# Optimization experiments

Hardware: AMD Instinct MI355X
Metric: run time of the kernel (lower is better)

## Reference

```python
import jax, jax.numpy as jnp
import numpy as np
import math

N_EMBD = 1024
N_HEAD = 16
HEAD_DIM = N_EMBD // N_HEAD


def setup_inputs() -> dict:
    key = jax.random.key(0)
    k_x, k_w1, k_b1, k_w2, k_b2 = jax.random.split(key, 5)
    B, T = 2, 2048
    x = jax.random.normal(k_x, (B, T, N_EMBD), dtype=jnp.float32)
    # ln1: Linear(n_embd, 3*n_embd); weights stored as [in, out] for x @ W
    W_qkv = jax.random.normal(k_w1, (N_EMBD, 3 * N_EMBD), dtype=jnp.float32) * 0.02
    b_qkv = jax.random.normal(k_b1, (3 * N_EMBD,), dtype=jnp.float32) * 0.02
    # ln2: Linear(n_embd, n_embd)
    W_out = jax.random.normal(k_w2, (N_EMBD, N_EMBD), dtype=jnp.float32) * 0.02
    b_out = jax.random.normal(k_b2, (N_EMBD,), dtype=jnp.float32) * 0.02
    return {"x": x, "W_qkv": W_qkv, "b_qkv": b_qkv, "W_out": W_out, "b_out": b_out}


def reference(x, W_qkv, b_qkv, W_out, b_out):
    B, T, C = x.shape
    qkv = x @ W_qkv + b_qkv                      # [B,T,3C]
    q, k, v = jnp.split(qkv, 3, axis=-1)
    # reshape to heads: [B, H, T, D]
    def to_heads(t):
        return t.reshape(B, T, N_HEAD, HEAD_DIM).transpose(0, 2, 1, 3)
    Q, K, V = to_heads(q), to_heads(k), to_heads(v)
    # NOTE: scale is 1/sqrt(n_head), as in the source (not sqrt(head_dim));
    # NOTE: no causal mask is applied, faithfully matching the source forward.
    scale = 1.0 / math.sqrt(N_HEAD)
    scores = jnp.einsum('bhqd,bhkd->bhqk', Q, K) * scale  # [B,H,T,T]
    attn = jax.nn.softmax(scores, axis=-1)
    out = jnp.einsum('bhqk,bhkd->bhqd', attn, V)          # [B,H,T,D]
    out = out.transpose(0, 2, 1, 3).reshape(B, T, C)
    # dropout = 0.0 -> identity (eval mode)
    return out @ W_out + b_out
```

## Files before the change

kernel.cpp:

```cpp
#include <hip/hip_runtime.h>
#include <hip/hip_bf16.h>
#include <stdint.h>

typedef __bf16 bf16_t;
typedef __bf16 bf16x8 __attribute__((ext_vector_type(8)));
typedef float  f32x4  __attribute__((ext_vector_type(4)));

#define AS1 __attribute__((address_space(1)))
#define AS3 __attribute__((address_space(3)))

__device__ __forceinline__ void gload16(const bf16_t* g, char* l) {
  __builtin_amdgcn_global_load_lds((AS1 const void*)(uintptr_t)g, (AS3 void*)l, 16, 0, 0);
}
__device__ __forceinline__ int swz8(int r) { return (r & 7) ^ ((r >> 2) & 6); }

#define C2S 0.36067376022224085f

__global__ void cvt_f32_bf16(const float* __restrict__ in, bf16_t* __restrict__ out, int n4) {
  int i = blockIdx.x * blockDim.x + threadIdx.x;
  if (i >= n4) return;
  float4 v = reinterpret_cast<const float4*>(in)[i];
  union { bf16_t h[4]; unsigned long long u; } r;
  r.h[0] = (bf16_t)v.x; r.h[1] = (bf16_t)v.y; r.h[2] = (bf16_t)v.z; r.h[3] = (bf16_t)v.w;
  reinterpret_cast<unsigned long long*>(out)[i] = r.u;
}

__global__ void trans_cvt(const float* __restrict__ W, bf16_t* __restrict__ Wt, int K, int N) {
  __shared__ float tile[32][33];
  const int kb = blockIdx.x * 32, nb = blockIdx.y * 32;
  const int tx = threadIdx.x, ty = threadIdx.y;
#pragma unroll
  for (int i = 0; i < 32; i += 8)
    tile[ty + i][tx] = W[(size_t)(kb + ty + i) * N + nb + tx];
  __syncthreads();
#pragma unroll
  for (int i = 0; i < 32; i += 8)
    Wt[(size_t)(nb + ty + i) * K + kb + tx] = (bf16_t)tile[tx][ty + i];
}

__global__ __launch_bounds__(256) void gemm_bt(
    const bf16_t* __restrict__ A, const bf16_t* __restrict__ Bt,
    const float* __restrict__ bias,
    bf16_t* __restrict__ outb, bf16_t* __restrict__ vtb, float* __restrict__ outf,
    int M, int N, int K, int ldo, int mode) {
  __shared__ bf16_t lA[128 * 32];
  __shared__ bf16_t lB[128 * 32];
  const int tid = threadIdx.x;
  const int wave = tid >> 6, lane = tid & 63;
  const int lr = lane & 15, lg = lane >> 4;
  const int ntiles = N >> 7;
  const int bid = (blockIdx.x & 7) * ((int)gridDim.x >> 3) + (blockIdx.x >> 3);
  const int bn = bid % ntiles, bm = bid / ntiles;
  const int m0 = bm * 128, n0 = bn * 128;
  const int wr = wave >> 1, wc = wave & 1;
  f32x4 acc[4][4] = {};

  for (int k0 = 0; k0 < K; k0 += 32) {
    __syncthreads();
#pragma unroll
    for (int it = 0; it < 2; ++it) {
      const int wbase = it * 256 + wave * 64;
      const int lam = wbase + lane;
      const int row = lam >> 2;
      const int colb = ((lam & 3) << 4) ^ (((row >> 1) & 3) << 4);
      gload16(A  + (size_t)(m0 + row) * K + k0 + (colb >> 1), (char*)lA + wbase * 16);
      gload16(Bt + (size_t)(n0 + row) * K + k0 + (colb >> 1), (char*)lB + wbase * 16);
    }
    __syncthreads();

    bf16x8 af[4], bfv[4];
#pragma unroll
    for (int mi = 0; mi < 4; ++mi) {
      const int row = wr * 64 + mi * 16 + lr;
      af[mi] = *reinterpret_cast<const bf16x8*>(
          (const char*)lA + row * 64 + ((lg * 16) ^ (((row >> 1) & 3) << 4)));
    }
#pragma unroll
    for (int ni = 0; ni < 4; ++ni) {
      const int row = wc * 64 + ni * 16 + lr;
      bfv[ni] = *reinterpret_cast<const bf16x8*>(
          (const char*)lB + row * 64 + ((lg * 16) ^ (((row >> 1) & 3) << 4)));
    }
    __builtin_amdgcn_s_setprio(1);
#pragma unroll
    for (int mi = 0; mi < 4; ++mi)
#pragma unroll
      for (int ni = 0; ni < 4; ++ni)
        acc[mi][ni] = __builtin_amdgcn_mfma_f32_16x16x32_bf16(af[mi], bfv[ni], acc[mi][ni], 0, 0, 0);
    __builtin_amdgcn_s_setprio(0);
  }

#pragma unroll
  for (int mi = 0; mi < 4; ++mi) {
#pragma unroll
    for (int ni = 0; ni < 4; ++ni) {
      const int col = n0 + wc * 64 + ni * 16 + lr;
      const float bv = bias[col];
      const int rg0 = m0 + wr * 64 + mi * 16 + lg * 4;
      if (mode == 1 && col >= 2048) {
        const int colv = col - 2048;
        const int dd = colv & 63, hh = colv >> 6;
        const int bb = rg0 >> 11, t = rg0 & 2047;
        union { bf16_t h4[4]; unsigned long long u; } pk;
#pragma unroll
        for (int r = 0; r < 4; ++r) pk.h4[r] = (bf16_t)(acc[mi][ni][r] + bv);
        *reinterpret_cast<unsigned long long*>(
            vtb + (size_t)(bb * 16 + hh) * 131072 + (size_t)dd * 2048 + t) = pk.u;
      } else {
        const float sc = (mode == 1 && col < 1024) ? C2S : 1.f;
#pragma unroll
        for (int r = 0; r < 4; ++r) {
          const float v = (acc[mi][ni][r] + bv) * sc;
          if (mode == 2) outf[(size_t)(rg0 + r) * ldo + col] = v;
          else           outb[(size_t)(rg0 + r) * ldo + col] = (bf16_t)v;
        }
      }
    }
  }
}

__global__ __launch_bounds__(512) void attn_fwd(
    const bf16_t* __restrict__ qkv2,
    const bf16_t* __restrict__ vT,
    bf16_t* __restrict__ a0, bf16_t* __restrict__ a1,
    float* __restrict__ lbuf) {
  __shared__ bf16_t lds[2][8192];
  const int tid = threadIdx.x;
  const int wave = tid >> 6, lane = tid & 63;
  const int lr = lane & 15, lg = lane >> 4;
  const int id = blockIdx.x;
  const int xcd = id & 7, slot = id >> 3;
  const int bh = xcd * 4 + (slot & 3);
  const int rest = slot >> 2;
  const int qb = rest & 7, kvh = rest >> 3;
  const int b = bh >> 4, h = bh & 15;

  const int q0 = qb * 256 + wave * 32;
  const bf16_t* Qp = qkv2 + (size_t)(b * 2048 + q0) * 2048 + h * 64;
  bf16x8 qf[2][2];
#pragma unroll
  for (int hx = 0; hx < 2; ++hx) {
    qf[hx][0] = *reinterpret_cast<const bf16x8*>(Qp + (size_t)(hx * 16 + lr) * 2048 + lg * 8);
    qf[hx][1] = *reinterpret_cast<const bf16x8*>(Qp + (size_t)(hx * 16 + lr) * 2048 + 32 + lg * 8);
  }

  const int kr = tid >> 3;
  const int ks = (tid & 7) ^ swz8(kr);
  const bf16_t* Ksrc = qkv2 + (size_t)(b * 2048 + kvh * 1024 + kr) * 2048 + 1024 + h * 64 + ks * 8;
  const bf16_t* Vsrc = vT + (size_t)bh * 131072 + (size_t)kr * 2048 + kvh * 1024 + ks * 8;

  auto stage = [&](int buf, int kb) {
    char* base = (char*)&lds[buf][0] + wave * 1024;
    gload16(Ksrc + (size_t)kb * 131072, base);
    gload16(Vsrc + (size_t)kb * 64, base + 8192);
  };

  int kofs[4][2], vofs[4][2];
#pragma unroll
  for (int t = 0; t < 4; ++t) {
    const int kk = 32 * (t >> 1) + 8 * (lr >> 2) + 4 * (t & 1) + (lr & 3);
    const int sw = swz8(kk) << 4;
    kofs[t][0] = (kk << 7) + ((lg * 16) ^ sw);
    kofs[t][1] = (kk << 7) + ((64 + lg * 16) ^ sw);
  }
#pragma unroll
  for (int nc = 0; nc < 4; ++nc) {
    const int vr = nc * 16 + lr;
    const int sw = swz8(vr) << 4;
    vofs[nc][0] = 8192 + (vr << 7) + ((lg * 16) ^ sw);
    vofs[nc][1] = 8192 + (vr << 7) + ((64 + lg * 16) ^ sw);
  }

  f32x4 acc[2][4] = {};
  f32x4 accl[2] = {};
  bf16x8 ones;
#pragma unroll
  for (int j = 0; j < 8; ++j) ones[j] = (bf16_t)1.0f;

  int cur = 0;
  stage(0, 0);
  __syncthreads();

  for (int kb = 0; kb < 16; ++kb) {
    if (kb < 15) stage(cur ^ 1, kb + 1);
    const char* bK = (const char*)&lds[cur][0];

    f32x4 s[2][4];
#pragma unroll
    for (int t = 0; t < 4; ++t) {
      const bf16x8 k0 = *reinterpret_cast<const bf16x8*>(bK + kofs[t][0]);
      const bf16x8 k1 = *reinterpret_cast<const bf16x8*>(bK + kofs[t][1]);
#pragma unroll
      for (int hx = 0; hx < 2; ++hx) {
        f32x4 z = {0.f, 0.f, 0.f, 0.f};
        z = __builtin_amdgcn_mfma_f32_16x16x32_bf16(k0, qf[hx][0], z, 0, 0, 0);
        s[hx][t] = __builtin_amdgcn_mfma_f32_16x16x32_bf16(k1, qf[hx][1], z, 0, 0, 0);
      }
    }

    bf16x8 pa[2][2];
#pragma unroll
    for (int hx = 0; hx < 2; ++hx) {
      float p[16];
#pragma unroll
      for (int t = 0; t < 4; ++t)
#pragma unroll
        for (int r = 0; r < 4; ++r)
          p[t * 4 + r] = __builtin_amdgcn_exp2f(s[hx][t][r]);
#pragma unroll
      for (int j = 0; j < 8; ++j) { pa[hx][0][j] = (bf16_t)p[j]; pa[hx][1][j] = (bf16_t)p[8 + j]; }
    }

    __builtin_amdgcn_s_setprio(1);
#pragma unroll
    for (int hx = 0; hx < 2; ++hx) {
      accl[hx] = __builtin_amdgcn_mfma_f32_16x16x32_bf16(pa[hx][0], ones, accl[hx], 0, 0, 0);
      accl[hx] = __builtin_amdgcn_mfma_f32_16x16x32_bf16(pa[hx][1], ones, accl[hx], 0, 0, 0);
    }

#pragma unroll
    for (int nc = 0; nc < 4; ++nc) {
      const bf16x8 v0 = *reinterpret_cast<const bf16x8*>(bK + vofs[nc][0]);
      const bf16x8 v1 = *reinterpret_cast<const bf16x8*>(bK + vofs[nc][1]);
#pragma unroll
      for (int hx = 0; hx < 2; ++hx) {
        acc[hx][nc] = __builtin_amdgcn_mfma_f32_16x16x32_bf16(pa[hx][0], v0, acc[hx][nc], 0, 0, 0);
        acc[hx][nc] = __builtin_amdgcn_mfma_f32_16x16x32_bf16(pa[hx][1], v1, acc[hx][nc], 0, 0, 0);
      }
    }
    __builtin_amdgcn_s_setprio(0);

    __syncthreads();
    cur ^= 1;
  }

  bf16_t* ap = kvh ? a1 : a0;
#pragma unroll
  for (int hx = 0; hx < 2; ++hx) {
#pragma unroll
    for (int r = 0; r < 4; ++r) {
      const float lf = 1.f / accl[hx][r];
      const int qg = q0 + hx * 16 + lg * 4 + r;
      bf16_t* op = ap + (size_t)(b * 2048 + qg) * 1024 + h * 64 + lr;
#pragma unroll
      for (int nc = 0; nc < 4; ++nc) op[nc * 16] = (bf16_t)(acc[hx][nc][r] * lf);
      if (lr == 0)
        lbuf[(size_t)(kvh * 4096 + b * 2048 + qg) * 16 + h] = accl[hx][r];
    }
  }
}

__global__ void attn_reduce(const bf16_t* __restrict__ a0, const bf16_t* __restrict__ a1,
                            const float* __restrict__ lbuf, bf16_t* __restrict__ aout) {
  const int i = blockIdx.x * 256 + threadIdx.x;
  const int r = i >> 7, h = (i & 127) >> 3;
  const float l0 = lbuf[(size_t)r * 16 + h];
  const float l1 = lbuf[(size_t)(4096 + r) * 16 + h];
  const float inv = 1.f / (l0 + l1);
  const float w0 = l0 * inv, w1 = l1 * inv;
  const bf16x8 v0 = reinterpret_cast<const bf16x8*>(a0)[i];
  const bf16x8 v1 = reinterpret_cast<const bf16x8*>(a1)[i];
  bf16x8 o;
#pragma unroll
  for (int j = 0; j < 8; ++j) o[j] = (bf16_t)(w0 * (float)v0[j] + w1 * (float)v1[j]);
  reinterpret_cast<bf16x8*>(aout)[i] = o;
}

extern "C" void kernel_launch(void* const* d_in, const int* in_sizes, int n_in,
                              void* d_out, int out_size, void* d_ws, size_t ws_size,
                              hipStream_t stream) {
  (void)in_sizes; (void)n_in; (void)out_size; (void)ws_size;
  const float* x    = (const float*)d_in[0];
  const float* Wqkv = (const float*)d_in[1];
  const float* bqkv = (const float*)d_in[2];
  const float* Wout = (const float*)d_in[3];
  const float* bout = (const float*)d_in[4];
  float* out = (float*)d_out;

  char* ws = (char*)d_ws;
  bf16_t* xb    = (bf16_t*)(ws);
  bf16_t* a0    = (bf16_t*)(ws);
  bf16_t* wqkvT = (bf16_t*)(ws + 8388608);
  bf16_t* woutT = (bf16_t*)(ws + 14680064);
  bf16_t* qkv2  = (bf16_t*)(ws + 16777216);
  bf16_t* aout  = (bf16_t*)(ws + 16777216);
  bf16_t* vT    = (bf16_t*)(ws + 33554432);
  bf16_t* a1    = (bf16_t*)(ws + 41943040);
  float*  lbuf  = (float*)(ws + 50331648);

  cvt_f32_bf16<<<4096, 256, 0, stream>>>(x, xb, 1048576);
  trans_cvt<<<dim3(32, 96), dim3(32, 8), 0, stream>>>(Wqkv, wqkvT, 1024, 3072);
  trans_cvt<<<dim3(32, 32), dim3(32, 8), 0, stream>>>(Wout, woutT, 1024, 1024);
  gemm_bt<<<768, 256, 0, stream>>>(xb, wqkvT, bqkv, qkv2, vT, nullptr, 4096, 3072, 1024, 2048, 1);
  attn_fwd<<<512, 512, 0, stream>>>(qkv2, vT, a0, a1, lbuf);
  attn_reduce<<<2048, 256, 0, stream>>>(a0, a1, lbuf, aout);
  gemm_bt<<<256, 256, 0, stream>>>(aout, woutT, bout, nullptr, nullptr, out, 4096, 1024, 1024, 1024, 2);
}
```

Measured before the change: 122.9 us.

## Fuse prep kernels, double-buffer GEMM LDS, and shrink out-proj tile

Merges the x conversion and both weight transpose-convert kernels into one prep launch. The GEMM now double-buffers its LDS tiles, so the next K slice is fetched while the current one goes through MFMA, with one barrier per iteration. The GEMM is templated on the M tile size, and the output projection uses 64-row tiles to launch 512 blocks instead of 256 and fill more CUs. In exchange, LDS use doubles and the smaller tile gives less data reuse in the output projection.

```diff
diff --git a/kernel.cpp b/kernel.cpp
--- a/kernel.cpp
+++ b/kernel.cpp
@@ -16,87 +16,111 @@
 
 #define C2S 0.36067376022224085f
 
-__global__ void cvt_f32_bf16(const float* __restrict__ in, bf16_t* __restrict__ out, int n4) {
-  int i = blockIdx.x * blockDim.x + threadIdx.x;
-  if (i >= n4) return;
-  float4 v = reinterpret_cast<const float4*>(in)[i];
-  union { bf16_t h[4]; unsigned long long u; } r;
-  r.h[0] = (bf16_t)v.x; r.h[1] = (bf16_t)v.y; r.h[2] = (bf16_t)v.z; r.h[3] = (bf16_t)v.w;
-  reinterpret_cast<unsigned long long*>(out)[i] = r.u;
-}
-
-__global__ void trans_cvt(const float* __restrict__ W, bf16_t* __restrict__ Wt, int K, int N) {
+__global__ __launch_bounds__(256) void prep(
+    const float* __restrict__ x, const float* __restrict__ Wqkv, const float* __restrict__ Wout,
+    bf16_t* __restrict__ xb, bf16_t* __restrict__ wqkvT, bf16_t* __restrict__ woutT) {
   __shared__ float tile[32][33];
-  const int kb = blockIdx.x * 32, nb = blockIdx.y * 32;
-  const int tx = threadIdx.x, ty = threadIdx.y;
+  const int bid = blockIdx.x, tid = threadIdx.x;
+  if (bid < 4096) {
+    const int i = bid * 256 + tid;
+    float4 v = reinterpret_cast<const float4*>(x)[i];
+    union { bf16_t h[4]; unsigned long long u; } r;
+    r.h[0] = (bf16_t)v.x; r.h[1] = (bf16_t)v.y; r.h[2] = (bf16_t)v.z; r.h[3] = (bf16_t)v.w;
+    reinterpret_cast<unsigned long long*>(xb)[i] = r.u;
+    return;
+  }
+  const float* W; bf16_t* Wt; int N, tb;
+  if (bid < 7168) { W = Wqkv; Wt = wqkvT; N = 3072; tb = bid - 4096; }
+  else            { W = Wout; Wt = woutT; N = 1024; tb = bid - 7168; }
+  const int kb = (tb & 31) * 32, nb = (tb >> 5) * 32;
+  const int tx = tid & 31, ty = tid >> 5;
 #pragma unroll
   for (int i = 0; i < 32; i += 8)
     tile[ty + i][tx] = W[(size_t)(kb + ty + i) * N + nb + tx];
   __syncthreads();
 #pragma unroll
   for (int i = 0; i < 32; i += 8)
-    Wt[(size_t)(nb + ty + i) * K + kb + tx] = (bf16_t)tile[tx][ty + i];
-}
-
+    Wt[(size_t)(nb + ty + i) * 1024 + kb + tx] = (bf16_t)tile[tx][ty + i];
+}
+
+template<int MI>
 __global__ __launch_bounds__(256) void gemm_bt(
     const bf16_t* __restrict__ A, const bf16_t* __restrict__ Bt,
     const float* __restrict__ bias,
     bf16_t* __restrict__ outb, bf16_t* __restrict__ vtb, float* __restrict__ outf,
     int M, int N, int K, int ldo, int mode) {
-  __shared__ bf16_t lA[128 * 32];
-  __shared__ bf16_t lB[128 * 32];
+  __shared__ bf16_t lA[2][MI * 1024];
+  __shared__ bf16_t lB[2][4096];
   const int tid = threadIdx.x;
   const int wave = tid >> 6, lane = tid & 63;
   const int lr = lane & 15, lg = lane >> 4;
   const int ntiles = N >> 7;
   const int bid = (blockIdx.x & 7) * ((int)gridDim.x >> 3) + (blockIdx.x >> 3);
   const int bn = bid % ntiles, bm = bid / ntiles;
-  const int m0 = bm * 128, n0 = bn * 128;
+  const int m0 = bm * (MI * 32), n0 = bn * 128;
   const int wr = wave >> 1, wc = wave & 1;
-  f32x4 acc[4][4] = {};
-
-  for (int k0 = 0; k0 < K; k0 += 32) {
-    __syncthreads();
+  f32x4 acc[MI][4] = {};
+
+  auto stageg = [&](int buf, int k0) {
+#pragma unroll
+    for (int it = 0; it < MI / 2; ++it) {
+      const int wbase = it * 256 + wave * 64;
+      const int lam = wbase + lane;
+      const int row = lam >> 2;
+      const int colb = ((lam & 3) << 4) ^ (((row >> 1) & 3) << 4);
+      gload16(A + (size_t)(m0 + row) * K + k0 + (colb >> 1), (char*)&lA[buf][0] + wbase * 16);
+    }
 #pragma unroll
     for (int it = 0; it < 2; ++it) {
       const int wbase = it * 256 + wave * 64;
       const int lam = wbase + lane;
       const int row = lam >> 2;
       const int colb = ((lam & 3) << 4) ^ (((row >> 1) & 3) << 4);
-      gload16(A  + (size_t)(m0 + row) * K + k0 + (colb >> 1), (char*)lA + wbase * 16);
-      gload16(Bt + (size_t)(n0 + row) * K + k0 + (colb >> 1), (char*)lB + wbase * 16);
-    }
-    __syncthreads();
-
-    bf16x8 af[4], bfv[4];
-#pragma unroll
-    for (int mi = 0; mi < 4; ++mi) {
-      const int row = wr * 64 + mi * 16 + lr;
+      gload16(Bt + (size_t)(n0 + row) * K + k0 + (colb >> 1), (char*)&lB[buf][0] + wbase * 16);
+    }
+  };
+
+  stageg(0, 0);
+  __syncthreads();
+  int cur = 0;
+
+  for (int k0 = 0; k0 < K; k0 += 32) {
+    if (k0 + 32 < K) stageg(cur ^ 1, k0 + 32);
+
+    const char* pA = (const char*)&lA[cur][0];
+    const char* pB = (const char*)&lB[cur][0];
+    bf16x8 af[MI], bfv[4];
+#pragma unroll
+    for (int mi = 0; mi < MI; ++mi) {
+      const int row = wr * (MI * 16) + mi * 16 + lr;
       af[mi] = *reinterpret_cast<const bf16x8*>(
-          (const char*)lA + row * 64 + ((lg * 16) ^ (((row >> 1) & 3) << 4)));
+          pA + row * 64 + ((lg * 16) ^ (((row >> 1) & 3) << 4)));
     }
 #pragma unroll
     for (int ni = 0; ni < 4; ++ni) {
       const int row = wc * 64 + ni * 16 + lr;
       bfv[ni] = *reinterpret_cast<const bf16x8*>(
-          (const char*)lB + row * 64 + ((lg * 16) ^ (((row >> 1) & 3) << 4)));
+          pB + row * 64 + ((lg * 16) ^ (((row >> 1) & 3) << 4)));
     }
     __builtin_amdgcn_s_setprio(1);
 #pragma unroll
-    for (int mi = 0; mi < 4; ++mi)
+    for (int mi = 0; mi < MI; ++mi)
 #pragma unroll
       for (int ni = 0; ni < 4; ++ni)
         acc[mi][ni] = __builtin_amdgcn_mfma_f32_16x16x32_bf16(af[mi], bfv[ni], acc[mi][ni], 0, 0, 0);
     __builtin_amdgcn_s_setprio(0);
-  }
-
-#pragma unroll
-  for (int mi = 0; mi < 4; ++mi) {
+
+    __syncthreads();
+    cur ^= 1;
+  }
+
+#pragma unroll
+  for (int mi = 0; mi < MI; ++mi) {
 #pragma unroll
     for (int ni = 0; ni < 4; ++ni) {
       const int col = n0 + wc * 64 + ni * 16 + lr;
       const float bv = bias[col];
-      const int rg0 = m0 + wr * 64 + mi * 16 + lg * 4;
+      const int rg0 = m0 + wr * (MI * 16) + mi * 16 + lg * 4;
       if (mode == 1 && col >= 2048) {
         const int colv = col - 2048;
         const int dd = colv & 63, hh = colv >> 6;
@@ -288,11 +312,9 @@
   bf16_t* a1    = (bf16_t*)(ws + 41943040);
   float*  lbuf  = (float*)(ws + 50331648);
 
-  cvt_f32_bf16<<<4096, 256, 0, stream>>>(x, xb, 1048576);
-  trans_cvt<<<dim3(32, 96), dim3(32, 8), 0, stream>>>(Wqkv, wqkvT, 1024, 3072);
-  trans_cvt<<<dim3(32, 32), dim3(32, 8), 0, stream>>>(Wout, woutT, 1024, 1024);
-  gemm_bt<<<768, 256, 0, stream>>>(xb, wqkvT, bqkv, qkv2, vT, nullptr, 4096, 3072, 1024, 2048, 1);
+  prep<<<8192, 256, 0, stream>>>(x, Wqkv, Wout, xb, wqkvT, woutT);
+  gemm_bt<4><<<768, 256, 0, stream>>>(xb, wqkvT, bqkv, qkv2, vT, nullptr, 4096, 3072, 1024, 2048, 1);
   attn_fwd<<<512, 512, 0, stream>>>(qkv2, vT, a0, a1, lbuf);
   attn_reduce<<<2048, 256, 0, stream>>>(a0, a1, lbuf, aout);
-  gemm_bt<<<256, 256, 0, stream>>>(aout, woutT, bout, nullptr, nullptr, out, 4096, 1024, 1024, 1024, 2);
-}
+  gemm_bt<2><<<512, 256, 0, stream>>>(aout, woutT, bout, nullptr, nullptr, out, 4096, 1024, 1024, 1024, 2);
+}
```

Measured after the change: 112.4 us. 8.6% less time.
